# Kernel tuning notes

Measured on AMD Instinct MI355X. Metric: run time of the kernel, lower is better.

## Reference

```python
import jax, jax.numpy as jnp
import numpy as np

TOL = 1e-5
CLIP_MAX = 1e5


def _mlp(z, W1, b1, W2, b2, W3, b3):
    # small per-edge MLP: 76 -> 32 -> 32 -> 1, scalar output per edge
    h1 = jax.nn.relu(z @ W1 + b1)
    h2 = jax.nn.relu(h1 @ W2 + b2)
    return (h2 @ W3 + b3)[..., 0]


def setup_inputs() -> dict:
    key = jax.random.key(0)
    ks = jax.random.split(key, 8)
    B, N, DH, DX, DE = 8, 256, 32, 3, 4
    D_IN = 2 * (DX + DH + 1) + DE  # 76
    h = jax.random.normal(ks[0], (B, N, DH), dtype=jnp.float32)
    e = jax.random.uniform(ks[1], (B, N, N, DE), dtype=jnp.float32)
    x = jax.random.normal(ks[2], (B, N, DX), dtype=jnp.float32)
    q = jax.random.normal(ks[3], (B, N, 1), dtype=jnp.float32)
    mask = jnp.ones((B, N, N, 1), dtype=jnp.float32)
    W1 = jax.random.normal(ks[4], (D_IN, 32), dtype=jnp.float32) * (1.0 / np.sqrt(D_IN))
    b1 = jnp.zeros((32,), dtype=jnp.float32)
    W2 = jax.random.normal(ks[5], (32, 32), dtype=jnp.float32) * (1.0 / np.sqrt(32))
    b2 = jnp.zeros((32,), dtype=jnp.float32)
    W3 = jax.random.normal(ks[6], (32, 1), dtype=jnp.float32) * (1.0 / np.sqrt(32))
    b3 = jnp.zeros((1,), dtype=jnp.float32)
    return {"h": h, "e": e, "x": x, "q": q, "mask": mask,
            "W1": W1, "b1": b1, "W2": W2, "b2": b2, "W3": W3, "b3": b3}


def reference(h, e, x, q, mask, W1, b1, W2, b2, W3, b3):
    T = 1
    B, N = e.shape[0], e.shape[1]
    clip = jnp.clip(e, TOL, CLIP_MAX)
    largest_e = jnp.max(clip, axis=-1)                      # [B,N,N]
    is_near = (largest_e != TOL).astype(jnp.float32)        # [B,N,N]
    mask_red = jnp.max(mask, axis=-1)                       # [B,N,N]
    for _ in range(T):
        inp_atom = jnp.concatenate([x, h, q], axis=-1)      # [B,N,D]
        D = inp_atom.shape[-1]
        inp_i = jnp.broadcast_to(inp_atom[:, :, None, :], (B, N, N, D))
        inp_j = jnp.transpose(inp_i, (0, 2, 1, 3))
        inp_ij = jnp.concatenate([inp_i, inp_j, e], axis=-1)  # [B,N,N,2D+De]
        inp_ji = jnp.concatenate([inp_j, inp_i, e], axis=-1)
        elec_ij = _mlp(inp_ij, W1, b1, W2, b2, W3, b3)      # [B,N,N]
        elec_ji = _mlp(inp_ji, W1, b1, W2, b2, W3, b3)
        antisym = 0.5 * (elec_ij - elec_ji) * mask_red * is_near
        q = q + jnp.sum(antisym, axis=2)[..., None]          # [B,N,1]
    return q
```

## Files before the change

### kernel.cpp

```cpp
#include <hip/hip_runtime.h>

#define TOL_F 1e-5f
#define CLIP_MAX_F 1e5f


__global__ __launch_bounds__(256) void precompute_kernel(
    const float* __restrict__ h,
    const float* __restrict__ x,
    const float* __restrict__ q,
    const float* __restrict__ W1,
    float* __restrict__ AT)
{
    const int gid = blockIdx.x * 256 + threadIdx.x;
    const int n  = gid >> 6;
    const int cc = gid & 63;
    const int b  = n >> 8;
    const int nl = n & 255;
    const int c  = cc & 31;
    const int rowbase = (cc < 32) ? 0 : 36;
    const float* Wcol = W1 + rowbase * 32 + c;

    const float* xp = x + n * 3;
    float acc = xp[0] * Wcol[0];
    acc = fmaf(xp[1], Wcol[32], acc);
    acc = fmaf(xp[2], Wcol[64], acc);
    const float* hp = h + n * 32;
    #pragma unroll
    for (int k = 0; k < 32; ++k)
        acc = fmaf(hp[k], Wcol[(3 + k) * 32], acc);
    acc = fmaf(q[n], Wcol[35 * 32], acc);

    AT[(b * 64 + cc) * 256 + nl] = acc;
}

__global__ __launch_bounds__(256) void edge_kernel(
    const float* __restrict__ e,
    const float* __restrict__ q,
    const float* __restrict__ mask,
    const float* __restrict__ W1,
    const float* __restrict__ b1,
    const float* __restrict__ W2,
    const float* __restrict__ b2,
    const float* __restrict__ W3,
    const float* __restrict__ AT,
    float* __restrict__ out)
{
    const int N = 256;
    const int b = blockIdx.x >> 8;
    const int i = blockIdx.x & 255;
    const int j = threadIdx.x;

    __shared__ float sW2T[32][33];
    __shared__ float sWe[4][32];
    __shared__ float sB1[32];
    __shared__ float sB2[32];
    __shared__ float sW3[32];
    __shared__ float sAI[64];
    __shared__ float sRed[4];

    for (int idx = threadIdx.x; idx < 32 * 32; idx += 256)
        sW2T[idx & 31][idx >> 5] = W2[idx];
    if (threadIdx.x < 128)
        sWe[threadIdx.x >> 5][threadIdx.x & 31] = W1[72 * 32 + threadIdx.x];
    if (threadIdx.x < 32) {
        sB1[threadIdx.x] = b1[threadIdx.x];
        sB2[threadIdx.x] = b2[threadIdx.x];
        sW3[threadIdx.x] = W3[threadIdx.x];
    }
    if (threadIdx.x < 64)
        sAI[threadIdx.x] = AT[(b * 64 + threadIdx.x) * 256 + i];
    __syncthreads();

    const int eoff = (b * N + i) * N + j;
    const float4 ev = ((const float4*)e)[eoff];
    const float m = mask[eoff];
    float c0 = fminf(fmaxf(ev.x, TOL_F), CLIP_MAX_F);
    float c1 = fminf(fmaxf(ev.y, TOL_F), CLIP_MAX_F);
    float c2 = fminf(fmaxf(ev.z, TOL_F), CLIP_MAX_F);
    float c3 = fminf(fmaxf(ev.w, TOL_F), CLIP_MAX_F);
    const float largest = fmaxf(fmaxf(c0, c1), fmaxf(c2, c3));
    const float nearf = (largest != TOL_F) ? 1.0f : 0.0f;

    const float* Ab = AT + b * 64 * 256 + j;
    float h1a[32], h1b[32];
    #pragma unroll
    for (int c = 0; c < 32; ++c) {
        float ew = sB1[c];
        ew = fmaf(ev.x, sWe[0][c], ew);
        ew = fmaf(ev.y, sWe[1][c], ew);
        ew = fmaf(ev.z, sWe[2][c], ew);
        ew = fmaf(ev.w, sWe[3][c], ew);
        const float alj = Ab[c * 256];
        const float ahj = Ab[(32 + c) * 256];
        h1a[c] = fmaxf(sAI[c] + ahj + ew, 0.0f);
        h1b[c] = fmaxf(alj + sAI[32 + c] + ew, 0.0f);
    }

    float outa = 0.0f, outb = 0.0f;
    #pragma unroll 4
    for (int c = 0; c < 32; ++c) {
        float acca = sB2[c], accb = sB2[c];
        #pragma unroll
        for (int k = 0; k < 32; ++k) {
            const float w = sW2T[c][k];
            acca = fmaf(h1a[k], w, acca);
            accb = fmaf(h1b[k], w, accb);
        }
        const float w3 = sW3[c];
        outa = fmaf(fmaxf(acca, 0.0f), w3, outa);
        outb = fmaf(fmaxf(accb, 0.0f), w3, outb);
    }

    float d = 0.5f * (outa - outb) * m * nearf;

    #pragma unroll
    for (int off = 32; off > 0; off >>= 1)
        d += __shfl_down(d, off, 64);
    const int lane = threadIdx.x & 63;
    const int wid = threadIdx.x >> 6;
    if (lane == 0) sRed[wid] = d;
    __syncthreads();
    if (threadIdx.x == 0) {
        const float s = sRed[0] + sRed[1] + sRed[2] + sRed[3];
        out[b * N + i] = q[b * N + i] + s;
    }
}

extern "C" void kernel_launch(void* const* d_in, const int* in_sizes, int n_in,
                              void* d_out, int out_size, void* d_ws, size_t ws_size,
                              hipStream_t stream) {
    const float* h    = (const float*)d_in[0];
    const float* e    = (const float*)d_in[1];
    const float* x    = (const float*)d_in[2];
    const float* q    = (const float*)d_in[3];
    const float* mask = (const float*)d_in[4];
    const float* W1   = (const float*)d_in[5];
    const float* b1   = (const float*)d_in[6];
    const float* W2   = (const float*)d_in[7];
    const float* b2   = (const float*)d_in[8];
    const float* W3   = (const float*)d_in[9];
    float* out = (float*)d_out;
    float* AT  = (float*)d_ws;

    hipLaunchKernelGGL(precompute_kernel, dim3(512), dim3(256), 0, stream,
                       h, x, q, W1, AT);
    hipLaunchKernelGGL(edge_kernel, dim3(8 * 256), dim3(256), 0, stream,
                       e, q, mask, W1, b1, W2, b2, W3, AT, out);
}
```

Before: 120.7 us.

## Compute edge MLP second layer with bf16 MFMA and node-major AT layout

Replaces the per-thread scalar 32x32 second-layer matmul with bf16 MFMA 16x16x32 instructions. Each wavefront handles 64 edges in four 16-edge tiles, and W2 is held in registers as bf16 B fragments. The precomputed per-node projections are stored node-major so each lane can load contiguous float4 chunks. This cuts the FP32 FMA work and register pressure from the 64-element h1 arrays, but rounds activations and weights to bf16, which adds precision error and extra shuffles to apply the per-edge scale.

```diff
diff --git a/kernel.cpp b/kernel.cpp
--- a/kernel.cpp
+++ b/kernel.cpp
@@ -1,8 +1,18 @@
 #include <hip/hip_runtime.h>
+#include <hip/hip_bf16.h>
 
 #define TOL_F 1e-5f
 #define CLIP_MAX_F 1e5f
 
+typedef __attribute__((ext_vector_type(8))) short v8s;
+typedef __attribute__((ext_vector_type(4))) float v4f;
+
+__device__ inline unsigned short f2bf(float f) {
+    __hip_bfloat16 t = __float2bfloat16(f);
+    union { __hip_bfloat16 b; unsigned short u; } cv;
+    cv.b = t;
+    return cv.u;
+}
 
 __global__ __launch_bounds__(256) void precompute_kernel(
     const float* __restrict__ h,
@@ -14,8 +24,6 @@
     const int gid = blockIdx.x * 256 + threadIdx.x;
     const int n  = gid >> 6;
     const int cc = gid & 63;
-    const int b  = n >> 8;
-    const int nl = n & 255;
     const int c  = cc & 31;
     const int rowbase = (cc < 32) ? 0 : 36;
     const float* Wcol = W1 + rowbase * 32 + c;
@@ -30,7 +38,7 @@
         acc = fmaf(hp[k], Wcol[(3 + k) * 32], acc);
     acc = fmaf(q[n], Wcol[35 * 32], acc);
 
-    AT[(b * 64 + cc) * 256 + nl] = acc;
+    AT[n * 64 + cc] = acc;
 }
 
 __global__ __launch_bounds__(256) void edge_kernel(
@@ -45,84 +53,101 @@
     const float* __restrict__ AT,
     float* __restrict__ out)
 {
-    const int N = 256;
     const int b = blockIdx.x >> 8;
     const int i = blockIdx.x & 255;
-    const int j = threadIdx.x;
+    const int lane = threadIdx.x & 63;
+    const int wv = threadIdx.x >> 6;
+    const int oc = lane & 15;
+    const int kg = lane >> 4;
+    const int c0 = kg * 8;
 
-    __shared__ float sW2T[32][33];
-    __shared__ float sWe[4][32];
-    __shared__ float sB1[32];
-    __shared__ float sB2[32];
-    __shared__ float sW3[32];
-    __shared__ float sAI[64];
-    __shared__ float sRed[4];
+    v8s B0, B1;
+    {
+        union { unsigned short u[8]; v8s v; } ub0, ub1;
+        #pragma unroll
+        for (int jj = 0; jj < 8; ++jj) {
+            ub0.u[jj] = f2bf(W2[(c0 + jj) * 32 + oc]);
+            ub1.u[jj] = f2bf(W2[(c0 + jj) * 32 + oc + 16]);
+        }
+        B0 = ub0.v; B1 = ub1.v;
+    }
+    const float b2a = b2[oc], b2b = b2[oc + 16];
+    const float w3a = W3[oc], w3b = W3[oc + 16];
 
-    for (int idx = threadIdx.x; idx < 32 * 32; idx += 256)
-        sW2T[idx & 31][idx >> 5] = W2[idx];
-    if (threadIdx.x < 128)
-        sWe[threadIdx.x >> 5][threadIdx.x & 31] = W1[72 * 32 + threadIdx.x];
-    if (threadIdx.x < 32) {
-        sB1[threadIdx.x] = b1[threadIdx.x];
-        sB2[threadIdx.x] = b2[threadIdx.x];
-        sW3[threadIdx.x] = W3[threadIdx.x];
-    }
-    if (threadIdx.x < 64)
-        sAI[threadIdx.x] = AT[(b * 64 + threadIdx.x) * 256 + i];
-    __syncthreads();
-
-    const int eoff = (b * N + i) * N + j;
-    const float4 ev = ((const float4*)e)[eoff];
-    const float m = mask[eoff];
-    float c0 = fminf(fmaxf(ev.x, TOL_F), CLIP_MAX_F);
-    float c1 = fminf(fmaxf(ev.y, TOL_F), CLIP_MAX_F);
-    float c2 = fminf(fmaxf(ev.z, TOL_F), CLIP_MAX_F);
-    float c3 = fminf(fmaxf(ev.w, TOL_F), CLIP_MAX_F);
-    const float largest = fmaxf(fmaxf(c0, c1), fmaxf(c2, c3));
-    const float nearf = (largest != TOL_F) ? 1.0f : 0.0f;
-
-    const float* Ab = AT + b * 64 * 256 + j;
-    float h1a[32], h1b[32];
+    const float* ATi = AT + (b * 256 + i) * 64;
+    float base_a[8], base_b[8];
+    float We[4][8];
     #pragma unroll
-    for (int c = 0; c < 32; ++c) {
-        float ew = sB1[c];
-        ew = fmaf(ev.x, sWe[0][c], ew);
-        ew = fmaf(ev.y, sWe[1][c], ew);
-        ew = fmaf(ev.z, sWe[2][c], ew);
-        ew = fmaf(ev.w, sWe[3][c], ew);
-        const float alj = Ab[c * 256];
-        const float ahj = Ab[(32 + c) * 256];
-        h1a[c] = fmaxf(sAI[c] + ahj + ew, 0.0f);
-        h1b[c] = fmaxf(alj + sAI[32 + c] + ew, 0.0f);
+    for (int jj = 0; jj < 8; ++jj) {
+        const float bb = b1[c0 + jj];
+        base_a[jj] = ATi[c0 + jj] + bb;
+        base_b[jj] = ATi[32 + c0 + jj] + bb;
+        #pragma unroll
+        for (int t = 0; t < 4; ++t)
+            We[t][jj] = W1[(72 + t) * 32 + c0 + jj];
     }
 
-    float outa = 0.0f, outb = 0.0f;
-    #pragma unroll 4
-    for (int c = 0; c < 32; ++c) {
-        float acca = sB2[c], accb = sB2[c];
+    const v4f Z = {0.f, 0.f, 0.f, 0.f};
+    float qacc = 0.f;
+
+    #pragma unroll
+    for (int t = 0; t < 4; ++t) {
+        const int jE = wv * 64 + t * 16 + oc;
+        const int eoff = (b * 256 + i) * 256 + jE;
+
+        const float4 ev = ((const float4*)e)[eoff];
+        const float m = mask[eoff];
+        const float cl0 = fminf(fmaxf(ev.x, TOL_F), CLIP_MAX_F);
+        const float cl1 = fminf(fmaxf(ev.y, TOL_F), CLIP_MAX_F);
+        const float cl2 = fminf(fmaxf(ev.z, TOL_F), CLIP_MAX_F);
+        const float cl3 = fminf(fmaxf(ev.w, TOL_F), CLIP_MAX_F);
+        const float largest = fmaxf(fmaxf(cl0, cl1), fmaxf(cl2, cl3));
+        const float nearf = (largest != TOL_F) ? 1.0f : 0.0f;
+        const float scale = 0.5f * m * nearf;
+
+        const float4* ATj4 = (const float4*)(AT + (b * 256 + jE) * 64);
+        const float4 lo0 = ATj4[kg * 2],     lo1 = ATj4[kg * 2 + 1];
+        const float4 hi0 = ATj4[8 + kg * 2], hi1 = ATj4[9 + kg * 2];
+        const float alo[8] = {lo0.x, lo0.y, lo0.z, lo0.w, lo1.x, lo1.y, lo1.z, lo1.w};
+        const float ahi[8] = {hi0.x, hi0.y, hi0.z, hi0.w, hi1.x, hi1.y, hi1.z, hi1.w};
+
+        union { unsigned short u[8]; v8s v; } ua, ub;
         #pragma unroll
-        for (int k = 0; k < 32; ++k) {
-            const float w = sW2T[c][k];
-            acca = fmaf(h1a[k], w, acca);
-            accb = fmaf(h1b[k], w, accb);
+        for (int jj = 0; jj < 8; ++jj) {
+            float ew = We[0][jj] * ev.x;
+            ew = fmaf(We[1][jj], ev.y, ew);
+            ew = fmaf(We[2][jj], ev.z, ew);
+            ew = fmaf(We[3][jj], ev.w, ew);
+            const float pa = base_a[jj] + ahi[jj] + ew;
+            const float pb = base_b[jj] + alo[jj] + ew;
+            ua.u[jj] = f2bf(fmaxf(pa, 0.f));
+            ub.u[jj] = f2bf(fmaxf(pb, 0.f));
         }
-        const float w3 = sW3[c];
-        outa = fmaf(fmaxf(acca, 0.0f), w3, outa);
-        outb = fmaf(fmaxf(accb, 0.0f), w3, outb);
+
+        v4f Da0 = __builtin_amdgcn_mfma_f32_16x16x32_bf16(ua.v, B0, Z, 0, 0, 0);
+        v4f Da1 = __builtin_amdgcn_mfma_f32_16x16x32_bf16(ua.v, B1, Z, 0, 0, 0);
+        v4f Db0 = __builtin_amdgcn_mfma_f32_16x16x32_bf16(ub.v, B0, Z, 0, 0, 0);
+        v4f Db1 = __builtin_amdgcn_mfma_f32_16x16x32_bf16(ub.v, B1, Z, 0, 0, 0);
+
+        #pragma unroll
+        for (int r = 0; r < 4; ++r) {
+            float va = fmaxf(Da1[r] + b2b, 0.f) * w3b;
+            va = fmaf(fmaxf(Da0[r] + b2a, 0.f), w3a, va);
+            float vb = fmaxf(Db1[r] + b2b, 0.f) * w3b;
+            vb = fmaf(fmaxf(Db0[r] + b2a, 0.f), w3a, vb);
+            const float sc = __shfl(scale, kg * 4 + r, 64);
+            qacc += (va - vb) * sc;
+        }
     }
-
-    float d = 0.5f * (outa - outb) * m * nearf;
 
     #pragma unroll
     for (int off = 32; off > 0; off >>= 1)
-        d += __shfl_down(d, off, 64);
-    const int lane = threadIdx.x & 63;
-    const int wid = threadIdx.x >> 6;
-    if (lane == 0) sRed[wid] = d;
+        qacc += __shfl_down(qacc, off, 64);
+    __shared__ float sRed[4];
+    if (lane == 0) sRed[wv] = qacc;
     __syncthreads();
     if (threadIdx.x == 0) {
-        const float s = sRed[0] + sRed[1] + sRed[2] + sRed[3];
-        out[b * N + i] = q[b * N + i] + s;
+        out[b * 256 + i] = q[b * 256 + i] + (sRed[0] + sRed[1] + sRed[2] + sRed[3]);
     }
 }
 
```

Measured after the change: 103.6 us. -14.2%, faster.
